# Performance work log

Hardware: AMD Instinct MI355X
Metric: run time of the kernel (lower is better)

Reference implementation:

```python
import jax, jax.numpy as jnp
import numpy as np

H, KVH, DH = 16, 4, 128
EPS = 1e-8

def _rmsnorm(t, gamma):
    # normalize over last dim (dim_head)
    ms = jnp.mean(t * t, axis=-1, keepdims=True)
    return t * jax.lax.rsqrt(ms + EPS) * gamma

def setup_inputs() -> dict:
    key = jax.random.key(0)
    ks = jax.random.split(key, 5)
    d = H * DH  # 2048
    kv_d = KVH * DH  # 512
    x = jax.random.normal(ks[0], (2, 2048, d), dtype=jnp.float32)
    Wq = jax.random.normal(ks[1], (d, d), dtype=jnp.float32) * (d ** -0.5)
    Wk = jax.random.normal(ks[2], (d, kv_d), dtype=jnp.float32) * (d ** -0.5)
    Wv = jax.random.normal(ks[3], (d, kv_d), dtype=jnp.float32) * (d ** -0.5)
    Wo = jax.random.normal(ks[4], (d, d), dtype=jnp.float32) * (d ** -0.5)
    q_gamma = jnp.ones((DH,), dtype=jnp.float32)
    k_gamma = jnp.ones((DH,), dtype=jnp.float32)
    return {"x": x, "Wq": Wq, "Wk": Wk, "Wv": Wv, "Wo": Wo,
            "q_gamma": q_gamma, "k_gamma": k_gamma}

def reference(x, Wq, Wk, Wv, Wo, q_gamma, k_gamma):
    b, s, d = x.shape
    g = H // KVH  # GQA group size
    q = (x @ Wq).reshape(b, s, H, DH)
    k = (x @ Wk).reshape(b, s, KVH, DH)
    v = (x @ Wv).reshape(b, s, KVH, DH)
    # fused QK RMSNorm (per-head, over dim_head)
    q = _rmsnorm(q, q_gamma)
    k = _rmsnorm(k, k_gamma)
    # GQA: expand kv heads across query-head groups
    k = jnp.repeat(k, g, axis=2)  # [b, s, H, DH]
    v = jnp.repeat(v, g, axis=2)
    scores = jnp.einsum('bqhd,bkhd->bhqk', q, k) * (DH ** -0.5)
    causal = jnp.tril(jnp.ones((s, s), dtype=bool))
    scores = jnp.where(causal, scores, jnp.finfo(scores.dtype).min)
    attn = jax.nn.softmax(scores, axis=-1)
    out = jnp.einsum('bhqk,bkhd->bqhd', attn, v).reshape(b, s, H * DH)
    out = out @ Wo
    return out + x  # residual skip
```

## Files before the change

kernel.cpp:

```cpp
#include <hip/hip_runtime.h>

typedef unsigned short u16;
typedef __attribute__((ext_vector_type(8))) short short8;
typedef __attribute__((ext_vector_type(4))) float f32x4;
typedef __attribute__((ext_vector_type(16))) float f32x16;

#define DEVI __device__ __forceinline__

DEVI float u2f(u16 u) {
    unsigned int x = ((unsigned int)u) << 16;
    float f; __builtin_memcpy(&f, &x, 4); return f;
}
DEVI u16 f2u(float f) {
    unsigned int x; __builtin_memcpy(&x, &f, 4);
    x = (x + 0x7fffu + ((x >> 16) & 1u)) >> 16;
    return (u16)x;
}
DEVI unsigned int fbits(float f) {
    unsigned int x; __builtin_memcpy(&x, &f, 4); return x;
}
DEVI unsigned int pkbf(float lo, float hi) {
    return __builtin_amdgcn_perm(fbits(hi), fbits(lo), 0x07060302u);
}
DEVI void gld16(const u16* g, u16* ldsbase) {
    __builtin_amdgcn_global_load_lds(
        (const __attribute__((address_space(1))) unsigned int*)g,
        (__attribute__((address_space(3))) unsigned int*)ldsbase, 16, 0, 0);
}

__global__ __launch_bounds__(256) void prep(
    const float* __restrict__ x,
    const float* __restrict__ Wq, const float* __restrict__ Wk,
    const float* __restrict__ Wv, const float* __restrict__ Wo,
    u16* __restrict__ xbf, u16* __restrict__ WTqkv, u16* __restrict__ WoT)
{
    __shared__ u16 T[64 * 72];
    int id = blockIdx.x;
    const int tid = threadIdx.x;
    if (id < 4096) {
        int g = (id * 256 + tid) * 8;
        float4 a = *(const float4*)&x[g];
        float4 c = *(const float4*)&x[g + 4];
        short8 v;
        v[0]=(short)f2u(a.x); v[1]=(short)f2u(a.y); v[2]=(short)f2u(a.z); v[3]=(short)f2u(a.w);
        v[4]=(short)f2u(c.x); v[5]=(short)f2u(c.y); v[6]=(short)f2u(c.z); v[7]=(short)f2u(c.w);
        *(short8*)&xbf[g] = v;
        return;
    }
    id -= 4096;
    const float* W; u16* WT; int N, bx, by;
    if (id < 1024)      {            W = Wo; WT = WoT;   N = 2048; bx = id & 31; by = id >> 5; }
    else if (id < 2048) { id -= 1024; W = Wq; WT = WTqkv; N = 2048; bx = id & 31; by = id >> 5; }
    else if (id < 2304) { id -= 2048; W = Wk; WT = WTqkv + (size_t)2048 * 2048; N = 512; bx = id & 7; by = id >> 3; }
    else                { id -= 2304; W = Wv; WT = WTqkv + (size_t)2560 * 2048; N = 512; bx = id & 7; by = id >> 3; }
    const int K = 2048;
    const int k0 = by * 64, n0 = bx * 64;
#pragma unroll
    for (int i = 0; i < 2; ++i) {
        int c = tid + i * 256;
        int row = c >> 3, n8 = (c & 7) * 8;
        const float* src = &W[(size_t)(k0 + row) * N + n0 + n8];
#pragma unroll
        for (int j = 0; j < 8; ++j)
            T[(n8 + j) * 72 + row] = f2u(src[j]);
    }
    __syncthreads();
#pragma unroll
    for (int i = 0; i < 2; ++i) {
        int c = tid + i * 256;
        int n = c >> 3, k8 = (c & 7) * 8;
        *(short8*)&WT[(size_t)(n0 + n) * K + k0 + k8] = *(const short8*)&T[n * 72 + k8];
    }
}

__global__ __launch_bounds__(256) void gemm_lds(
    const u16* __restrict__ A, int lda,
    const u16* __restrict__ WT,
    void* __restrict__ C, int ldc, const float* __restrict__ resid, int c_f32,
    int M, int N, int K,
    const float* __restrict__ qg, const float* __restrict__ kg, int fuse_norm)
{
    __shared__ u16 As[128 * 32];
    __shared__ u16 Bs[128 * 32];
    const int tid = threadIdx.x;
    const int lane = tid & 63, w = tid >> 6;
    const int wm = w >> 1, wn = w & 1;
    const int l15 = lane & 15, quad = lane >> 4;
    const int r4 = lane >> 2, c4 = (lane & 3) * 8;
    const int m0 = blockIdx.y * 128, n0 = blockIdx.x * 128;

    f32x4 acc[4][4] = {};
    for (int k0 = 0; k0 < K; k0 += 32) {
#pragma unroll
        for (int j = 0; j < 2; ++j) {
            int row = w * 32 + j * 16;
            gld16(&WT[(size_t)(n0 + row + r4) * K + k0 + c4], &Bs[row * 32]);
            gld16(&A [(size_t)(m0 + row + r4) * lda + k0 + c4], &As[row * 32]);
        }
        __syncthreads();
        short8 a[4], b[4];
#pragma unroll
        for (int mt = 0; mt < 4; ++mt)
            a[mt] = *(const short8*)&As[(wm * 64 + mt * 16 + l15) * 32 + quad * 8];
#pragma unroll
        for (int nt = 0; nt < 4; ++nt)
            b[nt] = *(const short8*)&Bs[(wn * 64 + nt * 16 + l15) * 32 + quad * 8];
#pragma unroll
        for (int mt = 0; mt < 4; ++mt)
#pragma unroll
            for (int nt = 0; nt < 4; ++nt)
                acc[mt][nt] = __builtin_amdgcn_mfma_f32_16x16x32_bf16(a[mt], b[nt], acc[mt][nt], 0, 0, 0);
        __syncthreads();
    }

    if (fuse_norm && n0 < 2560) {
        const float* gamma = (n0 < 2048) ? qg : kg;
        float* red = (float*)As;
#pragma unroll
        for (int mt = 0; mt < 4; ++mt)
#pragma unroll
            for (int r = 0; r < 4; ++r) {
                float p = 0.f;
#pragma unroll
                for (int nt = 0; nt < 4; ++nt) p += acc[mt][nt][r] * acc[mt][nt][r];
#pragma unroll
                for (int msk = 1; msk < 16; msk <<= 1) p += __shfl_xor(p, msk);
                if (l15 == 0)
                    red[(wm * 64 + mt * 16 + quad * 4 + r) * 2 + wn] = p;
            }
        __syncthreads();
        float gv[4];
#pragma unroll
        for (int nt = 0; nt < 4; ++nt) gv[nt] = gamma[wn * 64 + nt * 16 + l15];
#pragma unroll
        for (int mt = 0; mt < 4; ++mt)
#pragma unroll
            for (int r = 0; r < 4; ++r) {
                int rl = wm * 64 + mt * 16 + quad * 4 + r;
                float m2 = red[rl * 2] + red[rl * 2 + 1];
                float sc = rsqrtf(m2 * (1.0f / 128.0f) + 1e-8f);
#pragma unroll
                for (int nt = 0; nt < 4; ++nt) acc[mt][nt][r] *= sc * gv[nt];
            }
    }

#pragma unroll
    for (int mt = 0; mt < 4; ++mt) {
#pragma unroll
        for (int r = 0; r < 4; ++r) {
            int row = m0 + wm * 64 + mt * 16 + quad * 4 + r;
#pragma unroll
            for (int nt = 0; nt < 4; ++nt) {
                int col = n0 + wn * 64 + nt * 16 + l15;
                float v = acc[mt][nt][r];
                if (resid) v += resid[(size_t)row * ldc + col];
                if (c_f32) ((float*)C)[(size_t)row * ldc + col] = v;
                else       ((u16*)C)[(size_t)row * ldc + col] = f2u(v);
            }
        }
    }
}

__global__ __launch_bounds__(256) void vtrans(
    const u16* __restrict__ qkv, u16* __restrict__ vT)
{
    __shared__ u16 T[128 * 72];
    const int tid = threadIdx.x;
    const int t0 = blockIdx.x * 64;
    const int kvh = blockIdx.y, b = blockIdx.z;
#pragma unroll
    for (int i = 0; i < 4; ++i) {
        int c = tid + i * 256;
        int tl = c >> 4, d8 = (c & 15) * 8;
        short8 v = *(const short8*)&qkv[(size_t)(b * 2048 + t0 + tl) * 3072 + 2560 + kvh * 128 + d8];
#pragma unroll
        for (int j = 0; j < 8; ++j)
            T[(d8 + j) * 72 + tl] = (u16)v[j];
    }
    __syncthreads();
#pragma unroll
    for (int i = 0; i < 4; ++i) {
        int c = tid + i * 256;
        int d = c >> 3, t8 = (c & 7) * 8;
        *(short8*)&vT[((size_t)(b * 4 + kvh) * 128 + d) * 2048 + t0 + t8] =
            *(const short8*)&T[d * 72 + t8];
    }
}

#define SWZ(row, coloff) ((coloff) ^ (((row) & 7) << 4))
__global__ __launch_bounds__(256) void attn(
    u16* __restrict__ qkv, const u16* __restrict__ vT)
{
    __shared__ u16 lds[16384];
    char* const Kb = (char*)lds;
    char* const Vb = (char*)lds + 16384;

    const int tid = threadIdx.x, lane = tid & 63, w = tid >> 6;
    const int t = w >> 1, half = w & 1;
    const int l31 = lane & 31, h2 = lane >> 5;
    const int h = blockIdx.y, b = blockIdx.z;
    const int kvh = h >> 2;
    const int qts[2] = { (int)blockIdx.x, 31 - (int)blockIdx.x };
    const int qt = qts[t];
    const float scale = 0.08838834764831845f;

    short8 qf[8];
    {
        const u16* Qg = &qkv[(size_t)(b * 2048 + qt * 64 + half * 32 + l31) * 3072 + h * 128 + h2 * 8];
#pragma unroll
        for (int ks = 0; ks < 8; ++ks)
            qf[ks] = *(const short8*)&Qg[ks * 16];
    }

    f32x16 o2[4] = {};
    float m_ = -1e30f, l_ = 0.f;

    for (int kt = 0; kt <= qts[1]; ++kt) {
        const int kv0 = kt * 64;
#pragma unroll
        for (int i = 0; i < 4; ++i) {
            int c = tid + i * 256;
            int r = c >> 4, co = (c & 15) * 16;
            short8 v = *(const short8*)&qkv[(size_t)(b * 2048 + kv0 + r) * 3072 + 2048 + kvh * 128 + (c & 15) * 8];
            *(short8*)(Kb + r * 256 + SWZ(r, co)) = v;
        }
#pragma unroll
        for (int i = 0; i < 4; ++i) {
            int c = tid + i * 256;
            int d = c >> 3, co = (c & 7) * 16;
            short8 v = *(const short8*)&vT[((size_t)(b * 4 + kvh) * 128 + d) * 2048 + kv0 + (c & 7) * 8];
            *(short8*)(Vb + d * 128 + SWZ(d, co)) = v;
        }
        __syncthreads();

        if (kt <= qt) {
            f32x16 s2[2];
#pragma unroll
            for (int nt2 = 0; nt2 < 2; ++nt2) {
                f32x16 a = {};
                int row = nt2 * 32 + l31;
#pragma unroll
                for (int ks = 0; ks < 8; ++ks) {
                    short8 kf = *(const short8*)(Kb + row * 256 + SWZ(row, ks * 32 + h2 * 16));
                    a = __builtin_amdgcn_mfma_f32_32x32x16_bf16(kf, qf[ks], a, 0, 0, 0);
                }
                s2[nt2] = a;
            }
            if (kt == qt) {
                int qrow = half * 32 + l31;
#pragma unroll
                for (int nt2 = 0; nt2 < 2; ++nt2)
#pragma unroll
                    for (int r = 0; r < 16; ++r) {
                        int kvr = nt2 * 32 + (r & 3) + 8 * (r >> 2) + 4 * h2;
                        float v = s2[nt2][r] * scale;
                        if (kvr > qrow) v = -1e30f;
                        s2[nt2][r] = v;
                    }
            } else {
#pragma unroll
                for (int nt2 = 0; nt2 < 2; ++nt2)
#pragma unroll
                    for (int r = 0; r < 16; ++r) s2[nt2][r] *= scale;
            }
            float mx = s2[0][0];
#pragma unroll
            for (int nt2 = 0; nt2 < 2; ++nt2)
#pragma unroll
                for (int r = 0; r < 16; ++r) mx = fmaxf(mx, s2[nt2][r]);
            mx = fmaxf(mx, __shfl_xor(mx, 32));
            if (!__all(mx <= m_ + 8.0f)) {
                float mn = fmaxf(m_, mx);
                float alpha = __expf(m_ - mn);
                m_ = mn;
                l_ *= alpha;
#pragma unroll
                for (int r = 0; r < 16; ++r) {
                    float ar = __shfl(alpha, (r & 3) + 8 * (r >> 2) + 4 * h2);
#pragma unroll
                    for (int dblk = 0; dblk < 4; ++dblk) o2[dblk][r] *= ar;
                }
            }
            float sum = 0.f;
#pragma unroll
            for (int nt2 = 0; nt2 < 2; ++nt2)
#pragma unroll
                for (int r = 0; r < 16; ++r) {
                    float p = __expf(s2[nt2][r] - m_);
                    s2[nt2][r] = p;
                    sum += p;
                }
            sum += __shfl_xor(sum, 32);
            l_ += sum;
            short8 pa[4];
#pragma unroll
            for (int ch = 0; ch < 4; ++ch) {
                int nt2 = ch >> 1, cc = (ch & 1) * 8;
                unsigned int xa = pkbf(s2[nt2][cc + 0], s2[nt2][cc + 1]);
                unsigned int xb = pkbf(s2[nt2][cc + 2], s2[nt2][cc + 3]);
                unsigned int xc = pkbf(s2[nt2][cc + 4], s2[nt2][cc + 5]);
                unsigned int xd = pkbf(s2[nt2][cc + 6], s2[nt2][cc + 7]);
                unsigned int r1 = (unsigned int)__shfl_xor((int)(h2 ? xa : xc), 32);
                unsigned int r2 = (unsigned int)__shfl_xor((int)(h2 ? xb : xd), 32);
                union { unsigned int u[4]; short8 s8; } uu;
                uu.u[0] = h2 ? r1 : xa;
                uu.u[1] = h2 ? r2 : xb;
                uu.u[2] = h2 ? xc : r1;
                uu.u[3] = h2 ? xd : r2;
                pa[ch] = uu.s8;
            }
#pragma unroll
            for (int dblk = 0; dblk < 4; ++dblk) {
                int row = dblk * 32 + l31;
                f32x16 acc = o2[dblk];
#pragma unroll
                for (int ch = 0; ch < 4; ++ch) {
                    short8 bv = *(const short8*)(Vb + row * 128 + SWZ(row, ch * 32 + h2 * 16));
                    acc = __builtin_amdgcn_mfma_f32_32x32x16_bf16(pa[ch], bv, acc, 0, 0, 0);
                }
                o2[dblk] = acc;
            }
        }
        __syncthreads();
    }
    {
        float rl = 1.0f / l_;
#pragma unroll
        for (int r = 0; r < 16; ++r) {
            int qreg = (r & 3) + 8 * (r >> 2) + 4 * h2;
            float inv = __shfl(rl, qreg);
            int row = qt * 64 + half * 32 + qreg;
#pragma unroll
            for (int dblk = 0; dblk < 4; ++dblk)
                qkv[(size_t)(b * 2048 + row) * 3072 + h * 128 + dblk * 32 + l31] =
                    f2u(o2[dblk][r] * inv);
        }
    }
}

extern "C" void kernel_launch(void* const* d_in, const int* in_sizes, int n_in,
                              void* d_out, int out_size, void* d_ws, size_t ws_size,
                              hipStream_t stream) {
    const float* x  = (const float*)d_in[0];
    const float* Wq = (const float*)d_in[1];
    const float* Wk = (const float*)d_in[2];
    const float* Wv = (const float*)d_in[3];
    const float* Wo = (const float*)d_in[4];
    const float* qg = (const float*)d_in[5];
    const float* kg = (const float*)d_in[6];

    char* ws = (char*)d_ws;
    u16* WoT   = (u16*)(ws);
    u16* QKV   = (u16*)(ws + 8388608);
    u16* vT    = (u16*)(ws + 33554432);
    u16* WTqkv = (u16*)(ws + 33554432);
    u16* xbf   = (u16*)d_out;

    prep<<<dim3(6656), 256, 0, stream>>>(x, Wq, Wk, Wv, Wo, xbf, WTqkv, WoT);

    gemm_lds<<<dim3(24, 32), 256, 0, stream>>>(xbf, 2048, WTqkv, QKV, 3072,
                                               nullptr, 0, 4096, 3072, 2048,
                                               qg, kg, 1);

    vtrans<<<dim3(32, 4, 2), 256, 0, stream>>>(QKV, vT);

    attn<<<dim3(16, 16, 2), 256, 0, stream>>>(QKV, vT);

    gemm_lds<<<dim3(16, 32), 256, 0, stream>>>(QKV, 3072, WoT, d_out, 2048,
                                               x, 1, 4096, 2048, 2048,
                                               nullptr, nullptr, 0);
}
```

Baseline: 415.4 us.

## Stage Q in LDS and process attention in 32-wide KV sub-tiles

Q tiles for both query tiles are loaded once into a swizzled LDS buffer and re-read per MFMA instead of being held in eight register vectors. The score/softmax/PV path now runs per 32-column KV half-tile, keeping a single f32x16 score block and two packed P fragments live. On the diagonal tile it skips the fully masked upper half for the first warp half. This aims to cut VGPR pressure and wasted masked MFMA work, at the cost of doubling LDS per block (which can lower occupancy), extra LDS reads of Q, and one online-softmax rescale check per sub-tile instead of per tile.

Result: faster. 368.1 us (-11.4%).

```diff
diff --git a/kernel.cpp b/kernel.cpp
--- a/kernel.cpp
+++ b/kernel.cpp
@@ -191,31 +191,34 @@
 __global__ __launch_bounds__(256) void attn(
     u16* __restrict__ qkv, const u16* __restrict__ vT)
 {
-    __shared__ u16 lds[16384];
+    __shared__ u16 lds[32768];
     char* const Kb = (char*)lds;
     char* const Vb = (char*)lds + 16384;
+    char* const Qb = (char*)lds + 32768;
 
     const int tid = threadIdx.x, lane = tid & 63, w = tid >> 6;
     const int t = w >> 1, half = w & 1;
     const int l31 = lane & 31, h2 = lane >> 5;
     const int h = blockIdx.y, b = blockIdx.z;
     const int kvh = h >> 2;
-    const int qts[2] = { (int)blockIdx.x, 31 - (int)blockIdx.x };
-    const int qt = qts[t];
+    const int qts0 = (int)blockIdx.x, qts1 = 31 - (int)blockIdx.x;
+    const int qt = t ? qts1 : qts0;
     const float scale = 0.08838834764831845f;
 
-    short8 qf[8];
-    {
-        const u16* Qg = &qkv[(size_t)(b * 2048 + qt * 64 + half * 32 + l31) * 3072 + h * 128 + h2 * 8];
-#pragma unroll
-        for (int ks = 0; ks < 8; ++ks)
-            qf[ks] = *(const short8*)&Qg[ks * 16];
-    }
+#pragma unroll
+    for (int i = 0; i < 8; ++i) {
+        int c = tid + i * 256;
+        int r = c >> 4, co = (c & 15) * 16;
+        int qtile = (r >> 6) ? qts1 : qts0;
+        short8 v = *(const short8*)&qkv[(size_t)(b * 2048 + qtile * 64 + (r & 63)) * 3072 + h * 128 + (c & 15) * 8];
+        *(short8*)(Qb + r * 256 + SWZ(r, co)) = v;
+    }
+    const int myqrow = t * 64 + half * 32 + l31;
 
     f32x16 o2[4] = {};
     float m_ = -1e30f, l_ = 0.f;
 
-    for (int kt = 0; kt <= qts[1]; ++kt) {
+    for (int kt = 0; kt <= qts1; ++kt) {
         const int kv0 = kt * 64;
 #pragma unroll
         for (int i = 0; i < 4; ++i) {
@@ -234,91 +237,81 @@
         __syncthreads();
 
         if (kt <= qt) {
-            f32x16 s2[2];
 #pragma unroll
             for (int nt2 = 0; nt2 < 2; ++nt2) {
-                f32x16 a = {};
-                int row = nt2 * 32 + l31;
+                if (kt == qt && half == 0 && nt2 == 1) continue;
+                f32x16 s = {};
+                int krow = nt2 * 32 + l31;
 #pragma unroll
                 for (int ks = 0; ks < 8; ++ks) {
-                    short8 kf = *(const short8*)(Kb + row * 256 + SWZ(row, ks * 32 + h2 * 16));
-                    a = __builtin_amdgcn_mfma_f32_32x32x16_bf16(kf, qf[ks], a, 0, 0, 0);
-                }
-                s2[nt2] = a;
-            }
-            if (kt == qt) {
-                int qrow = half * 32 + l31;
-#pragma unroll
-                for (int nt2 = 0; nt2 < 2; ++nt2)
+                    short8 kf = *(const short8*)(Kb + krow * 256 + SWZ(krow, ks * 32 + h2 * 16));
+                    short8 qf = *(const short8*)(Qb + myqrow * 256 + SWZ(myqrow, ks * 32 + h2 * 16));
+                    s = __builtin_amdgcn_mfma_f32_32x32x16_bf16(kf, qf, s, 0, 0, 0);
+                }
+                if (kt == qt) {
+                    int qrow = half * 32 + l31;
 #pragma unroll
                     for (int r = 0; r < 16; ++r) {
                         int kvr = nt2 * 32 + (r & 3) + 8 * (r >> 2) + 4 * h2;
-                        float v = s2[nt2][r] * scale;
+                        float v = s[r] * scale;
                         if (kvr > qrow) v = -1e30f;
-                        s2[nt2][r] = v;
+                        s[r] = v;
                     }
-            } else {
-#pragma unroll
-                for (int nt2 = 0; nt2 < 2; ++nt2)
-#pragma unroll
-                    for (int r = 0; r < 16; ++r) s2[nt2][r] *= scale;
-            }
-            float mx = s2[0][0];
-#pragma unroll
-            for (int nt2 = 0; nt2 < 2; ++nt2)
-#pragma unroll
-                for (int r = 0; r < 16; ++r) mx = fmaxf(mx, s2[nt2][r]);
-            mx = fmaxf(mx, __shfl_xor(mx, 32));
-            if (!__all(mx <= m_ + 8.0f)) {
-                float mn = fmaxf(m_, mx);
-                float alpha = __expf(m_ - mn);
-                m_ = mn;
-                l_ *= alpha;
+                } else {
+#pragma unroll
+                    for (int r = 0; r < 16; ++r) s[r] *= scale;
+                }
+                float mx = s[0];
+#pragma unroll
+                for (int r = 1; r < 16; ++r) mx = fmaxf(mx, s[r]);
+                mx = fmaxf(mx, __shfl_xor(mx, 32));
+                if (!__all(mx <= m_ + 8.0f)) {
+                    float mn = fmaxf(m_, mx);
+                    float alpha = __expf(m_ - mn);
+                    m_ = mn;
+                    l_ *= alpha;
+#pragma unroll
+                    for (int r = 0; r < 16; ++r) {
+                        float ar = __shfl(alpha, (r & 3) + 8 * (r >> 2) + 4 * h2);
+#pragma unroll
+                        for (int dblk = 0; dblk < 4; ++dblk) o2[dblk][r] *= ar;
+                    }
+                }
+                float sum = 0.f;
 #pragma unroll
                 for (int r = 0; r < 16; ++r) {
-                    float ar = __shfl(alpha, (r & 3) + 8 * (r >> 2) + 4 * h2);
-#pragma unroll
-                    for (int dblk = 0; dblk < 4; ++dblk) o2[dblk][r] *= ar;
-                }
-            }
-            float sum = 0.f;
-#pragma unroll
-            for (int nt2 = 0; nt2 < 2; ++nt2)
-#pragma unroll
-                for (int r = 0; r < 16; ++r) {
-                    float p = __expf(s2[nt2][r] - m_);
-                    s2[nt2][r] = p;
+                    float p = __expf(s[r] - m_);
+                    s[r] = p;
                     sum += p;
                 }
-            sum += __shfl_xor(sum, 32);
-            l_ += sum;
-            short8 pa[4];
-#pragma unroll
-            for (int ch = 0; ch < 4; ++ch) {
-                int nt2 = ch >> 1, cc = (ch & 1) * 8;
-                unsigned int xa = pkbf(s2[nt2][cc + 0], s2[nt2][cc + 1]);
-                unsigned int xb = pkbf(s2[nt2][cc + 2], s2[nt2][cc + 3]);
-                unsigned int xc = pkbf(s2[nt2][cc + 4], s2[nt2][cc + 5]);
-                unsigned int xd = pkbf(s2[nt2][cc + 6], s2[nt2][cc + 7]);
-                unsigned int r1 = (unsigned int)__shfl_xor((int)(h2 ? xa : xc), 32);
-                unsigned int r2 = (unsigned int)__shfl_xor((int)(h2 ? xb : xd), 32);
-                union { unsigned int u[4]; short8 s8; } uu;
-                uu.u[0] = h2 ? r1 : xa;
-                uu.u[1] = h2 ? r2 : xb;
-                uu.u[2] = h2 ? xc : r1;
-                uu.u[3] = h2 ? xd : r2;
-                pa[ch] = uu.s8;
-            }
-#pragma unroll
-            for (int dblk = 0; dblk < 4; ++dblk) {
-                int row = dblk * 32 + l31;
-                f32x16 acc = o2[dblk];
-#pragma unroll
-                for (int ch = 0; ch < 4; ++ch) {
-                    short8 bv = *(const short8*)(Vb + row * 128 + SWZ(row, ch * 32 + h2 * 16));
-                    acc = __builtin_amdgcn_mfma_f32_32x32x16_bf16(pa[ch], bv, acc, 0, 0, 0);
-                }
-                o2[dblk] = acc;
+                sum += __shfl_xor(sum, 32);
+                l_ += sum;
+                short8 pa[2];
+#pragma unroll
+                for (int cc = 0; cc < 2; ++cc) {
+                    unsigned int xa = pkbf(s[cc * 8 + 0], s[cc * 8 + 1]);
+                    unsigned int xb = pkbf(s[cc * 8 + 2], s[cc * 8 + 3]);
+                    unsigned int xc = pkbf(s[cc * 8 + 4], s[cc * 8 + 5]);
+                    unsigned int xd = pkbf(s[cc * 8 + 6], s[cc * 8 + 7]);
+                    unsigned int r1 = (unsigned int)__shfl_xor((int)(h2 ? xa : xc), 32);
+                    unsigned int r2 = (unsigned int)__shfl_xor((int)(h2 ? xb : xd), 32);
+                    union { unsigned int u[4]; short8 s8; } uu;
+                    uu.u[0] = h2 ? r1 : xa;
+                    uu.u[1] = h2 ? r2 : xb;
+                    uu.u[2] = h2 ? xc : r1;
+                    uu.u[3] = h2 ? xd : r2;
+                    pa[cc] = uu.s8;
+                }
+#pragma unroll
+                for (int dblk = 0; dblk < 4; ++dblk) {
+                    int vrow = dblk * 32 + l31;
+                    f32x16 acc = o2[dblk];
+                    short8 bv0 = *(const short8*)(Vb + vrow * 128 + SWZ(vrow, nt2 * 64 + h2 * 16));
+                    acc = __builtin_amdgcn_mfma_f32_32x32x16_bf16(pa[0], bv0, acc, 0, 0, 0);
+                    short8 bv1 = *(const short8*)(Vb + vrow * 128 + SWZ(vrow, nt2 * 64 + 32 + h2 * 16));
+                    acc = __builtin_amdgcn_mfma_f32_32x32x16_bf16(pa[1], bv1, acc, 0, 0, 0);
+                    o2[dblk] = acc;
+                }
             }
         }
         __syncthreads();
```
